# Kernel optimization log

Measured on AMD Instinct MI355X. Metric: run time of the kernel, lower is better.

## Reference

```python
import jax, jax.numpy as jnp
import numpy as np

EPS = 1e-5


def setup_inputs() -> dict:
    key = jax.random.key(0)
    ks = jax.random.split(key, 12)
    B, T, F = 8192, 512, 4
    IN = F + 1          # market features + prev_delta
    H = 32              # lstm hidden
    D1 = 32             # decision mlp width
    s = 0.1
    return {
        "x": jax.random.normal(ks[0], (B, T, F), dtype=jnp.float32),
        # BatchNorm1d (inference mode: running stats)
        "bn_gamma": jnp.ones((IN,), jnp.float32),
        "bn_beta": jnp.zeros((IN,), jnp.float32),
        "bn_mean": jnp.zeros((IN,), jnp.float32),
        "bn_var": jnp.ones((IN,), jnp.float32),
        # LSTMCell params, gate order i,f,g,o (torch convention)
        "W_ih": jax.random.normal(ks[1], (4 * H, IN), jnp.float32) * s,
        "b_ih": jax.random.normal(ks[2], (4 * H,), jnp.float32) * s,
        "W_hh": jax.random.normal(ks[3], (4 * H, H), jnp.float32) * s,
        "b_hh": jax.random.normal(ks[4], (4 * H,), jnp.float32) * s,
        # decision MLP: Linear(H,32) -> ReLU -> Linear(32,1) -> Sigmoid
        "W1": jax.random.normal(ks[5], (D1, H), jnp.float32) * s,
        "b1": jax.random.normal(ks[6], (D1,), jnp.float32) * s,
        "W2": jax.random.normal(ks[7], (1, D1), jnp.float32) * s,
        "b2": jax.random.normal(ks[8], (1,), jnp.float32) * s,
    }


def reference(x, bn_gamma, bn_beta, bn_mean, bn_var,
              W_ih, b_ih, W_hh, b_hh, W1, b1, W2, b2):
    B, T, F = x.shape
    H = W_hh.shape[1]
    inv_std = jax.lax.rsqrt(bn_var + EPS)

    def step(carry, x_t):
        h, c, d = carry                                  # [B,H],[B,H],[B,1]
        z = jnp.concatenate([x_t, d], axis=1)            # [B, F+1]
        z = (z - bn_mean) * inv_std * bn_gamma + bn_beta
        gates = z @ W_ih.T + b_ih + h @ W_hh.T + b_hh    # [B, 4H]
        i, f, g, o = jnp.split(gates, 4, axis=1)
        c = jax.nn.sigmoid(f) * c + jax.nn.sigmoid(i) * jnp.tanh(g)
        h = jax.nn.sigmoid(o) * jnp.tanh(c)
        d = jax.nn.sigmoid(jax.nn.relu(h @ W1.T + b1) @ W2.T + b2)  # [B,1]
        return (h, c, d), d

    init = (jnp.zeros((B, H), x.dtype),
            jnp.zeros((B, H), x.dtype),
            jnp.zeros((B, 1), x.dtype))
    _, deltas = jax.lax.scan(step, init, jnp.swapaxes(x, 0, 1))  # [T,B,1]
    return jnp.swapaxes(deltas, 0, 1)                             # [B,T,1]
```

## Files before the change

kernel.cpp:

```cpp
#include <hip/hip_runtime.h>
#include <math.h>

#define T_STEPS 512
#define NF 4
#define HID 32
#define BN_EPS 1e-5f
#define LOG2E 1.44269504088896340736f

typedef float    f32x2 __attribute__((ext_vector_type(2)));
typedef float    f32x4 __attribute__((ext_vector_type(4)));
typedef _Float16 f16x2 __attribute__((ext_vector_type(2)));
typedef _Float16 f16x8 __attribute__((ext_vector_type(8)));

struct F8 { f16x2 p[4]; };

__device__ __forceinline__ f16x2 pk16(float x, float y) {
  return __builtin_bit_cast(f16x2, __builtin_amdgcn_cvt_pkrtz(x, y));
}
__device__ __forceinline__ f16x8 mk8(f16x2 a, f16x2 b, f16x2 c, f16x2 d) {
  F8 f; f.p[0] = a; f.p[1] = b; f.p[2] = c; f.p[3] = d;
  return __builtin_bit_cast(f16x8, f);
}
#if __has_builtin(__builtin_amdgcn_exp2f)
__device__ __forceinline__ float ex2(float x) { return __builtin_amdgcn_exp2f(x); }
#else
__device__ __forceinline__ float ex2(float x) { return exp2f(x); }
#endif
__device__ __forceinline__ float fsigmoid(float x) {
  return __builtin_amdgcn_rcpf(1.0f + __expf(-x));
}
__device__ __forceinline__ f32x4 mfma16(f16x8 a, f16x8 b, f32x4 c) {
  return __builtin_amdgcn_mfma_f32_16x16x32_f16(a, b, c, 0, 0, 0);
}

__global__ __launch_bounds__(256, 2) void hedge_kernel(
    const float* __restrict__ x,
    const float* __restrict__ bn_g, const float* __restrict__ bn_b,
    const float* __restrict__ bn_m, const float* __restrict__ bn_v,
    const float* __restrict__ W_ih, const float* __restrict__ b_ih,
    const float* __restrict__ W_hh, const float* __restrict__ b_hh,
    const float* __restrict__ W1,   const float* __restrict__ b1,
    const float* __restrict__ W2,   const float* __restrict__ b2,
    float* __restrict__ out)
{
  __shared__ f32x4 sact[2][4][2][4][16];

  const int tid  = threadIdx.x;
  const int lane = tid & 63;
  const int w    = tid >> 6;
  const int n    = lane & 15;
  const int q    = lane >> 4;
  const int row  = blockIdx.x * 16 + n;

  float scale[5], shift[5];
  #pragma unroll
  for (int f = 0; f < 5; ++f) {
    float s = bn_g[f] * rsqrtf(bn_v[f] + BN_EPS);
    scale[f] = s;
    shift[f] = fmaf(-bn_m[f], s, bn_b[f]);
  }

  const float ke = (w == 2) ? -2.0f * LOG2E : -LOG2E;
  const float aA = (w == 2) ?  2.0f : 1.0f;
  const float bA = (w == 2) ? -1.0f : 0.0f;

  const f16x2 zz = {(_Float16)0, (_Float16)0};

  f16x8 Ahh[2], Aih[2];
  f32x4 Cb[2], Wd[2];
  #pragma unroll
  for (int pp = 0; pp < 2; ++pp) {
    const int g = 2 * w + pp;
    const float* Wr = &W_hh[(16 * g + n) * HID];
    const f32x4 lo = *(const f32x4*)&Wr[4 * q];
    const f32x4 hi = *(const f32x4*)&Wr[16 + 4 * q];
    Ahh[pp] = mk8(pk16(ke * lo.x, ke * lo.y), pk16(ke * lo.z, ke * lo.w),
                  pk16(ke * hi.x, ke * hi.y), pk16(ke * hi.z, ke * hi.w));
    const float* Wi = &W_ih[(16 * g + n) * 5];
    Aih[pp] = mk8(q == 0 ? pk16(ke * Wi[0] * scale[0], ke * Wi[1] * scale[1]) : zz,
                  q == 0 ? pk16(ke * Wi[2] * scale[2], ke * Wi[3] * scale[3]) : zz,
                  zz, zz);
    #pragma unroll
    for (int r2 = 0; r2 < 4; ++r2) {
      const int rr = 16 * g + 4 * q + r2;
      float a = b_ih[rr] + b_hh[rr];
      #pragma unroll
      for (int f = 0; f < 5; ++f) a = fmaf(W_ih[rr * 5 + f], shift[f], a);
      Cb[pp][r2] = ke * a;
      Wd[pp][r2] = ke * W_ih[rr * 5 + 4] * scale[4];
    }
  }
  f16x8 Aw1[2];
  f32x4 Cb1[2], W2v[2];
  #pragma unroll
  for (int p = 0; p < 2; ++p) {
    const float* Wr = &W1[(16 * p + n) * HID];
    const f32x4 lo = *(const f32x4*)&Wr[4 * q];
    const f32x4 hi = *(const f32x4*)&Wr[16 + 4 * q];
    Aw1[p] = mk8(pk16(lo.x, lo.y), pk16(lo.z, lo.w),
                 pk16(hi.x, hi.y), pk16(hi.z, hi.w));
    #pragma unroll
    for (int r2 = 0; r2 < 4; ++r2) {
      Cb1[p][r2] = b1[16 * p + 4 * q + r2];
      W2v[p][r2] = W2[16 * p + 4 * q + r2];
    }
  }
  const float b2s = b2[0];

  const float* xrow = x + (size_t)row * (T_STEPS * NF);
  float*       orow = out + (size_t)row * T_STEPS;

  float cst0[4] = {0, 0, 0, 0}, cst1[4] = {0, 0, 0, 0};
  f16x8 Bh = mk8(zz, zz, zz, zz);
  f32x4 xv = *(const f32x4*)xrow;

  #pragma unroll 1
  for (int t = 0; t < T_STEPS; ++t) {
    const int tn = (t + 1 < T_STEPS) ? t + 1 : t;
    const f32x4 xn = *(const f32x4*)(xrow + tn * NF);
    const int bsel = t & 1;

    const f16x8 Bz = mk8(q == 0 ? pk16(xv.x, xv.y) : zz,
                         q == 0 ? pk16(xv.z, xv.w) : zz, zz, zz);
    f32x4 D0 = mfma16(Aih[0], Bz, mfma16(Ahh[0], Bh, Cb[0]));
    f32x4 D1 = mfma16(Aih[1], Bz, mfma16(Ahh[1], Bh, Cb[1]));
    const f32x4 M0 = mfma16(Aw1[0], Bh, Cb1[0]);
    const f32x4 M1 = mfma16(Aw1[1], Bh, Cb1[1]);

    float y = 0.0f;
    #pragma unroll
    for (int r2 = 0; r2 < 4; ++r2) {
      y = fmaf(W2v[0][r2], fmaxf(M0[r2], 0.0f), y);
      y = fmaf(W2v[1][r2], fmaxf(M1[r2], 0.0f), y);
    }
    y += __builtin_bit_cast(float, __builtin_amdgcn_ds_swizzle(
             __builtin_bit_cast(int, y), 0x401F));
    y += __shfl_xor(y, 32);
    float dl = fsigmoid(y + b2s);
    dl = t ? dl : 0.0f;
    if (w == 0 && q == 0 && t) orow[t - 1] = dl;

    f32x4 A0, A1;
    #pragma unroll
    for (int r2 = 0; r2 < 4; ++r2) {
      const float d0 = fmaf(Wd[0][r2], dl, D0[r2]);
      const float d1 = fmaf(Wd[1][r2], dl, D1[r2]);
      A0[r2] = fmaf(aA, __builtin_amdgcn_rcpf(1.0f + ex2(d0)), bA);
      A1[r2] = fmaf(aA, __builtin_amdgcn_rcpf(1.0f + ex2(d1)), bA);
    }

    sact[bsel][w][0][q][n] = A0;
    sact[bsel][w][1][q][n] = A1;
    __syncthreads();
    const f32x4 Iv0 = sact[bsel][0][0][q][n], Iv1 = sact[bsel][0][1][q][n];
    const f32x4 Fv0 = sact[bsel][1][0][q][n], Fv1 = sact[bsel][1][1][q][n];
    const f32x4 Gv0 = sact[bsel][2][0][q][n], Gv1 = sact[bsel][2][1][q][n];
    const f32x4 Ov0 = sact[bsel][3][0][q][n], Ov1 = sact[bsel][3][1][q][n];

    float hN[8];
    #pragma unroll
    for (int r2 = 0; r2 < 4; ++r2) {
      float cc0 = fmaf(Fv0[r2], cst0[r2], Iv0[r2] * Gv0[r2]);
      float cc1 = fmaf(Fv1[r2], cst1[r2], Iv1[r2] * Gv1[r2]);
      cst0[r2] = cc0; cst1[r2] = cc1;
      const float tc0 = fmaf(2.0f, __builtin_amdgcn_rcpf(1.0f + ex2(-2.0f * LOG2E * cc0)), -1.0f);
      const float tc1 = fmaf(2.0f, __builtin_amdgcn_rcpf(1.0f + ex2(-2.0f * LOG2E * cc1)), -1.0f);
      hN[r2]     = Ov0[r2] * tc0;
      hN[4 + r2] = Ov1[r2] * tc1;
    }
    Bh = mk8(pk16(hN[0], hN[1]), pk16(hN[2], hN[3]),
             pk16(hN[4], hN[5]), pk16(hN[6], hN[7]));
    xv = xn;
  }

  const f32x4 M0 = mfma16(Aw1[0], Bh, Cb1[0]);
  const f32x4 M1 = mfma16(Aw1[1], Bh, Cb1[1]);
  float y = 0.0f;
  #pragma unroll
  for (int r2 = 0; r2 < 4; ++r2) {
    y = fmaf(W2v[0][r2], fmaxf(M0[r2], 0.0f), y);
    y = fmaf(W2v[1][r2], fmaxf(M1[r2], 0.0f), y);
  }
  y += __builtin_bit_cast(float, __builtin_amdgcn_ds_swizzle(
           __builtin_bit_cast(int, y), 0x401F));
  y += __shfl_xor(y, 32);
  const float dl = fsigmoid(y + b2s);
  if (w == 0 && q == 0) orow[T_STEPS - 1] = dl;
}

extern "C" void kernel_launch(void* const* d_in, const int* in_sizes, int n_in,
                              void* d_out, int out_size, void* d_ws, size_t ws_size,
                              hipStream_t stream) {
  const float* x    = (const float*)d_in[0];
  const float* bn_g = (const float*)d_in[1];
  const float* bn_b = (const float*)d_in[2];
  const float* bn_m = (const float*)d_in[3];
  const float* bn_v = (const float*)d_in[4];
  const float* W_ih = (const float*)d_in[5];
  const float* b_ih = (const float*)d_in[6];
  const float* W_hh = (const float*)d_in[7];
  const float* b_hh = (const float*)d_in[8];
  const float* W1   = (const float*)d_in[9];
  const float* b1   = (const float*)d_in[10];
  const float* W2   = (const float*)d_in[11];
  const float* b2   = (const float*)d_in[12];
  float* out = (float*)d_out;

  const int B = in_sizes[0] / (T_STEPS * NF);
  const int grid = B / 16;

  hipLaunchKernelGGL(hedge_kernel, dim3(grid), dim3(256), 0, stream,
                     x, bn_g, bn_b, bn_m, bn_v, W_ih, b_ih, W_hh, b_hh,
                     W1, b1, W2, b2, out);
}
```

Baseline: 558.7 us.

## Split LSTM gate work across eight waves and distribute the cell update per element

Doubles the block to 512 threads so each wave computes one 16-row gate slice with a single MFMA chain, where before each wave computed two. The cell and hidden update now assigns one hidden element per thread instead of eight replicated per lane. The new hidden state is exchanged through a shared buffer and re-packed into the MFMA B operand. The aim is to shorten the serial per-step critical path and raise waves per CU. The cost is a second block-wide barrier per timestep and the loss of the double-buffered activation array.

Measured after the change: 525.6 us. -5.9%, faster.

```diff
diff --git a/kernel.cpp b/kernel.cpp
--- a/kernel.cpp
+++ b/kernel.cpp
@@ -7,7 +7,6 @@
 #define BN_EPS 1e-5f
 #define LOG2E 1.44269504088896340736f
 
-typedef float    f32x2 __attribute__((ext_vector_type(2)));
 typedef float    f32x4 __attribute__((ext_vector_type(4)));
 typedef _Float16 f16x2 __attribute__((ext_vector_type(2)));
 typedef _Float16 f16x8 __attribute__((ext_vector_type(8)));
@@ -33,7 +32,7 @@
   return __builtin_amdgcn_mfma_f32_16x16x32_f16(a, b, c, 0, 0, 0);
 }
 
-__global__ __launch_bounds__(256, 2) void hedge_kernel(
+__global__ __launch_bounds__(512, 4) void hedge_kernel(
     const float* __restrict__ x,
     const float* __restrict__ bn_g, const float* __restrict__ bn_b,
     const float* __restrict__ bn_m, const float* __restrict__ bn_v,
@@ -43,7 +42,8 @@
     const float* __restrict__ W2,   const float* __restrict__ b2,
     float* __restrict__ out)
 {
-  __shared__ f32x4 sact[2][4][2][4][16];
+  __shared__ f32x4 sact[8][4][16];
+  __shared__ __align__(16) float sh[16][36];
 
   const int tid  = threadIdx.x;
   const int lane = tid & 63;
@@ -51,6 +51,7 @@
   const int n    = lane & 15;
   const int q    = lane >> 4;
   const int row  = blockIdx.x * 16 + n;
+  const int gate = w >> 1;
 
   float scale[5], shift[5];
   #pragma unroll
@@ -60,34 +61,32 @@
     shift[f] = fmaf(-bn_m[f], s, bn_b[f]);
   }
 
-  const float ke = (w == 2) ? -2.0f * LOG2E : -LOG2E;
-  const float aA = (w == 2) ?  2.0f : 1.0f;
-  const float bA = (w == 2) ? -1.0f : 0.0f;
+  const float ke = (gate == 2) ? -2.0f * LOG2E : -LOG2E;
+  const float aA = (gate == 2) ?  2.0f : 1.0f;
+  const float bA = (gate == 2) ? -1.0f : 0.0f;
 
   const f16x2 zz = {(_Float16)0, (_Float16)0};
 
-  f16x8 Ahh[2], Aih[2];
-  f32x4 Cb[2], Wd[2];
-  #pragma unroll
-  for (int pp = 0; pp < 2; ++pp) {
-    const int g = 2 * w + pp;
-    const float* Wr = &W_hh[(16 * g + n) * HID];
+  f16x8 Ahh, Aih;
+  f32x4 Cb, Wd;
+  {
+    const float* Wr = &W_hh[(16 * w + n) * HID];
     const f32x4 lo = *(const f32x4*)&Wr[4 * q];
     const f32x4 hi = *(const f32x4*)&Wr[16 + 4 * q];
-    Ahh[pp] = mk8(pk16(ke * lo.x, ke * lo.y), pk16(ke * lo.z, ke * lo.w),
-                  pk16(ke * hi.x, ke * hi.y), pk16(ke * hi.z, ke * hi.w));
-    const float* Wi = &W_ih[(16 * g + n) * 5];
-    Aih[pp] = mk8(q == 0 ? pk16(ke * Wi[0] * scale[0], ke * Wi[1] * scale[1]) : zz,
-                  q == 0 ? pk16(ke * Wi[2] * scale[2], ke * Wi[3] * scale[3]) : zz,
-                  zz, zz);
-    #pragma unroll
-    for (int r2 = 0; r2 < 4; ++r2) {
-      const int rr = 16 * g + 4 * q + r2;
+    Ahh = mk8(pk16(ke * lo.x, ke * lo.y), pk16(ke * lo.z, ke * lo.w),
+              pk16(ke * hi.x, ke * hi.y), pk16(ke * hi.z, ke * hi.w));
+    const float* Wi = &W_ih[(16 * w + n) * 5];
+    Aih = mk8(q == 0 ? pk16(ke * Wi[0] * scale[0], ke * Wi[1] * scale[1]) : zz,
+              q == 0 ? pk16(ke * Wi[2] * scale[2], ke * Wi[3] * scale[3]) : zz,
+              zz, zz);
+    #pragma unroll
+    for (int r2 = 0; r2 < 4; ++r2) {
+      const int rr = 16 * w + 4 * q + r2;
       float a = b_ih[rr] + b_hh[rr];
       #pragma unroll
       for (int f = 0; f < 5; ++f) a = fmaf(W_ih[rr * 5 + f], shift[f], a);
-      Cb[pp][r2] = ke * a;
-      Wd[pp][r2] = ke * W_ih[rr * 5 + 4] * scale[4];
+      Cb[r2] = ke * a;
+      Wd[r2] = ke * W_ih[rr * 5 + 4] * scale[4];
     }
   }
   f16x8 Aw1[2];
@@ -107,10 +106,14 @@
   }
   const float b2s = b2[0];
 
+  const float* sA   = (const float*)sact;
+  const int ibase   = (((w >> 2) * 4 + (w & 3)) * 16 + n) * 4 + q;
+  const int hwrite  = 4 * w + q;
+
   const float* xrow = x + (size_t)row * (T_STEPS * NF);
   float*       orow = out + (size_t)row * T_STEPS;
 
-  float cst0[4] = {0, 0, 0, 0}, cst1[4] = {0, 0, 0, 0};
+  float ccur = 0.0f;
   f16x8 Bh = mk8(zz, zz, zz, zz);
   f32x4 xv = *(const f32x4*)xrow;
 
@@ -118,12 +121,10 @@
   for (int t = 0; t < T_STEPS; ++t) {
     const int tn = (t + 1 < T_STEPS) ? t + 1 : t;
     const f32x4 xn = *(const f32x4*)(xrow + tn * NF);
-    const int bsel = t & 1;
 
     const f16x8 Bz = mk8(q == 0 ? pk16(xv.x, xv.y) : zz,
                          q == 0 ? pk16(xv.z, xv.w) : zz, zz, zz);
-    f32x4 D0 = mfma16(Aih[0], Bz, mfma16(Ahh[0], Bh, Cb[0]));
-    f32x4 D1 = mfma16(Aih[1], Bz, mfma16(Ahh[1], Bh, Cb[1]));
+    f32x4 D = mfma16(Aih, Bz, mfma16(Ahh, Bh, Cb));
     const f32x4 M0 = mfma16(Aw1[0], Bh, Cb1[0]);
     const f32x4 M1 = mfma16(Aw1[1], Bh, Cb1[1]);
 
@@ -140,36 +141,31 @@
     dl = t ? dl : 0.0f;
     if (w == 0 && q == 0 && t) orow[t - 1] = dl;
 
-    f32x4 A0, A1;
-    #pragma unroll
-    for (int r2 = 0; r2 < 4; ++r2) {
-      const float d0 = fmaf(Wd[0][r2], dl, D0[r2]);
-      const float d1 = fmaf(Wd[1][r2], dl, D1[r2]);
-      A0[r2] = fmaf(aA, __builtin_amdgcn_rcpf(1.0f + ex2(d0)), bA);
-      A1[r2] = fmaf(aA, __builtin_amdgcn_rcpf(1.0f + ex2(d1)), bA);
-    }
-
-    sact[bsel][w][0][q][n] = A0;
-    sact[bsel][w][1][q][n] = A1;
+    f32x4 A;
+    #pragma unroll
+    for (int r2 = 0; r2 < 4; ++r2) {
+      const float dd = fmaf(Wd[r2], dl, D[r2]);
+      A[r2] = fmaf(aA, __builtin_amdgcn_rcpf(1.0f + ex2(dd)), bA);
+    }
+
+    sact[w][q][n] = A;
     __syncthreads();
-    const f32x4 Iv0 = sact[bsel][0][0][q][n], Iv1 = sact[bsel][0][1][q][n];
-    const f32x4 Fv0 = sact[bsel][1][0][q][n], Fv1 = sact[bsel][1][1][q][n];
-    const f32x4 Gv0 = sact[bsel][2][0][q][n], Gv1 = sact[bsel][2][1][q][n];
-    const f32x4 Ov0 = sact[bsel][3][0][q][n], Ov1 = sact[bsel][3][1][q][n];
-
-    float hN[8];
-    #pragma unroll
-    for (int r2 = 0; r2 < 4; ++r2) {
-      float cc0 = fmaf(Fv0[r2], cst0[r2], Iv0[r2] * Gv0[r2]);
-      float cc1 = fmaf(Fv1[r2], cst1[r2], Iv1[r2] * Gv1[r2]);
-      cst0[r2] = cc0; cst1[r2] = cc1;
-      const float tc0 = fmaf(2.0f, __builtin_amdgcn_rcpf(1.0f + ex2(-2.0f * LOG2E * cc0)), -1.0f);
-      const float tc1 = fmaf(2.0f, __builtin_amdgcn_rcpf(1.0f + ex2(-2.0f * LOG2E * cc1)), -1.0f);
-      hN[r2]     = Ov0[r2] * tc0;
-      hN[4 + r2] = Ov1[r2] * tc1;
-    }
-    Bh = mk8(pk16(hN[0], hN[1]), pk16(hN[2], hN[3]),
-             pk16(hN[4], hN[5]), pk16(hN[6], hN[7]));
+
+    const float iv = sA[ibase];
+    const float fv = sA[ibase + 512];
+    const float gv = sA[ibase + 1024];
+    const float ov = sA[ibase + 1536];
+    const float cc = fmaf(fv, ccur, iv * gv);
+    ccur = cc;
+    const float tc = fmaf(2.0f,
+        __builtin_amdgcn_rcpf(1.0f + ex2(-2.0f * LOG2E * cc)), -1.0f);
+    sh[n][hwrite] = ov * tc;
+
+    __syncthreads();
+    const f32x4 hlo = *(const f32x4*)&sh[n][4 * q];
+    const f32x4 hhi = *(const f32x4*)&sh[n][16 + 4 * q];
+    Bh = mk8(pk16(hlo.x, hlo.y), pk16(hlo.z, hlo.w),
+             pk16(hhi.x, hhi.y), pk16(hhi.z, hhi.w));
     xv = xn;
   }
 
@@ -209,7 +205,7 @@
   const int B = in_sizes[0] / (T_STEPS * NF);
   const int grid = B / 16;
 
-  hipLaunchKernelGGL(hedge_kernel, dim3(grid), dim3(256), 0, stream,
+  hipLaunchKernelGGL(hedge_kernel, dim3(grid), dim3(512), 0, stream,
                      x, bn_g, bn_b, bn_m, bn_v, W_ih, b_ih, W_hh, b_hh,
                      W1, b1, W2, b2, out);
 }
```

## Compute all LSTM gate tiles in one wave, removing LDS exchange and barrier

Applied to the files above, without the earlier changes.

Each block is reduced from four waves to one wave, which now computes all eight gate MFMA tiles and their activations itself. This removes the per-step shared-memory exchange of gate activations and the __syncthreads barrier. In exchange, each wave does four times the MFMA and transcendental work per step, and total resident waves drop fourfold, reducing parallelism across SIMDs.

New measurement: 519.3 us. -7.1%, faster.

```diff
diff --git a/kernel.cpp b/kernel.cpp
--- a/kernel.cpp
+++ b/kernel.cpp
@@ -7,7 +7,6 @@
 #define BN_EPS 1e-5f
 #define LOG2E 1.44269504088896340736f
 
-typedef float    f32x2 __attribute__((ext_vector_type(2)));
 typedef float    f32x4 __attribute__((ext_vector_type(4)));
 typedef _Float16 f16x2 __attribute__((ext_vector_type(2)));
 typedef _Float16 f16x8 __attribute__((ext_vector_type(8)));
@@ -33,7 +32,7 @@
   return __builtin_amdgcn_mfma_f32_16x16x32_f16(a, b, c, 0, 0, 0);
 }
 
-__global__ __launch_bounds__(256, 2) void hedge_kernel(
+__global__ __launch_bounds__(64, 1) void hedge_kernel(
     const float* __restrict__ x,
     const float* __restrict__ bn_g, const float* __restrict__ bn_b,
     const float* __restrict__ bn_m, const float* __restrict__ bn_v,
@@ -43,11 +42,7 @@
     const float* __restrict__ W2,   const float* __restrict__ b2,
     float* __restrict__ out)
 {
-  __shared__ f32x4 sact[2][4][2][4][16];
-
-  const int tid  = threadIdx.x;
-  const int lane = tid & 63;
-  const int w    = tid >> 6;
+  const int lane = threadIdx.x & 63;
   const int n    = lane & 15;
   const int q    = lane >> 4;
   const int row  = blockIdx.x * 16 + n;
@@ -60,34 +55,30 @@
     shift[f] = fmaf(-bn_m[f], s, bn_b[f]);
   }
 
-  const float ke = (w == 2) ? -2.0f * LOG2E : -LOG2E;
-  const float aA = (w == 2) ?  2.0f : 1.0f;
-  const float bA = (w == 2) ? -1.0f : 0.0f;
-
   const f16x2 zz = {(_Float16)0, (_Float16)0};
 
-  f16x8 Ahh[2], Aih[2];
-  f32x4 Cb[2], Wd[2];
-  #pragma unroll
-  for (int pp = 0; pp < 2; ++pp) {
-    const int g = 2 * w + pp;
-    const float* Wr = &W_hh[(16 * g + n) * HID];
+  f16x8 Ahh[8], Aih[8];
+  f32x4 Cb[8], Wd[8];
+  #pragma unroll
+  for (int tl = 0; tl < 8; ++tl) {
+    const float ke = (tl == 4 || tl == 5) ? -2.0f * LOG2E : -LOG2E;
+    const float* Wr = &W_hh[(16 * tl + n) * HID];
     const f32x4 lo = *(const f32x4*)&Wr[4 * q];
     const f32x4 hi = *(const f32x4*)&Wr[16 + 4 * q];
-    Ahh[pp] = mk8(pk16(ke * lo.x, ke * lo.y), pk16(ke * lo.z, ke * lo.w),
+    Ahh[tl] = mk8(pk16(ke * lo.x, ke * lo.y), pk16(ke * lo.z, ke * lo.w),
                   pk16(ke * hi.x, ke * hi.y), pk16(ke * hi.z, ke * hi.w));
-    const float* Wi = &W_ih[(16 * g + n) * 5];
-    Aih[pp] = mk8(q == 0 ? pk16(ke * Wi[0] * scale[0], ke * Wi[1] * scale[1]) : zz,
+    const float* Wi = &W_ih[(16 * tl + n) * 5];
+    Aih[tl] = mk8(q == 0 ? pk16(ke * Wi[0] * scale[0], ke * Wi[1] * scale[1]) : zz,
                   q == 0 ? pk16(ke * Wi[2] * scale[2], ke * Wi[3] * scale[3]) : zz,
                   zz, zz);
     #pragma unroll
     for (int r2 = 0; r2 < 4; ++r2) {
-      const int rr = 16 * g + 4 * q + r2;
+      const int rr = 16 * tl + 4 * q + r2;
       float a = b_ih[rr] + b_hh[rr];
       #pragma unroll
       for (int f = 0; f < 5; ++f) a = fmaf(W_ih[rr * 5 + f], shift[f], a);
-      Cb[pp][r2] = ke * a;
-      Wd[pp][r2] = ke * W_ih[rr * 5 + 4] * scale[4];
+      Cb[tl][r2] = ke * a;
+      Wd[tl][r2] = ke * W_ih[rr * 5 + 4] * scale[4];
     }
   }
   f16x8 Aw1[2];
@@ -110,7 +101,7 @@
   const float* xrow = x + (size_t)row * (T_STEPS * NF);
   float*       orow = out + (size_t)row * T_STEPS;
 
-  float cst0[4] = {0, 0, 0, 0}, cst1[4] = {0, 0, 0, 0};
+  float cst[8] = {0, 0, 0, 0, 0, 0, 0, 0};
   f16x8 Bh = mk8(zz, zz, zz, zz);
   f32x4 xv = *(const f32x4*)xrow;
 
@@ -118,12 +109,13 @@
   for (int t = 0; t < T_STEPS; ++t) {
     const int tn = (t + 1 < T_STEPS) ? t + 1 : t;
     const f32x4 xn = *(const f32x4*)(xrow + tn * NF);
-    const int bsel = t & 1;
 
     const f16x8 Bz = mk8(q == 0 ? pk16(xv.x, xv.y) : zz,
                          q == 0 ? pk16(xv.z, xv.w) : zz, zz, zz);
-    f32x4 D0 = mfma16(Aih[0], Bz, mfma16(Ahh[0], Bh, Cb[0]));
-    f32x4 D1 = mfma16(Aih[1], Bz, mfma16(Ahh[1], Bh, Cb[1]));
+    f32x4 D[8];
+    #pragma unroll
+    for (int tl = 0; tl < 8; ++tl)
+      D[tl] = mfma16(Aih[tl], Bz, mfma16(Ahh[tl], Bh, Cb[tl]));
     const f32x4 M0 = mfma16(Aw1[0], Bh, Cb1[0]);
     const f32x4 M1 = mfma16(Aw1[1], Bh, Cb1[1]);
 
@@ -138,35 +130,32 @@
     y += __shfl_xor(y, 32);
     float dl = fsigmoid(y + b2s);
     dl = t ? dl : 0.0f;
-    if (w == 0 && q == 0 && t) orow[t - 1] = dl;
-
-    f32x4 A0, A1;
-    #pragma unroll
-    for (int r2 = 0; r2 < 4; ++r2) {
-      const float d0 = fmaf(Wd[0][r2], dl, D0[r2]);
-      const float d1 = fmaf(Wd[1][r2], dl, D1[r2]);
-      A0[r2] = fmaf(aA, __builtin_amdgcn_rcpf(1.0f + ex2(d0)), bA);
-      A1[r2] = fmaf(aA, __builtin_amdgcn_rcpf(1.0f + ex2(d1)), bA);
-    }
-
-    sact[bsel][w][0][q][n] = A0;
-    sact[bsel][w][1][q][n] = A1;
-    __syncthreads();
-    const f32x4 Iv0 = sact[bsel][0][0][q][n], Iv1 = sact[bsel][0][1][q][n];
-    const f32x4 Fv0 = sact[bsel][1][0][q][n], Fv1 = sact[bsel][1][1][q][n];
-    const f32x4 Gv0 = sact[bsel][2][0][q][n], Gv1 = sact[bsel][2][1][q][n];
-    const f32x4 Ov0 = sact[bsel][3][0][q][n], Ov1 = sact[bsel][3][1][q][n];
+    if (q == 0 && t) orow[t - 1] = dl;
+
+    f32x4 Ac[8];
+    #pragma unroll
+    for (int tl = 0; tl < 8; ++tl) {
+      #pragma unroll
+      for (int r2 = 0; r2 < 4; ++r2) {
+        const float dd = fmaf(Wd[tl][r2], dl, D[tl][r2]);
+        const float rc = __builtin_amdgcn_rcpf(1.0f + ex2(dd));
+        Ac[tl][r2] = (tl == 4 || tl == 5) ? fmaf(2.0f, rc, -1.0f) : rc;
+      }
+    }
 
     float hN[8];
     #pragma unroll
-    for (int r2 = 0; r2 < 4; ++r2) {
-      float cc0 = fmaf(Fv0[r2], cst0[r2], Iv0[r2] * Gv0[r2]);
-      float cc1 = fmaf(Fv1[r2], cst1[r2], Iv1[r2] * Gv1[r2]);
-      cst0[r2] = cc0; cst1[r2] = cc1;
-      const float tc0 = fmaf(2.0f, __builtin_amdgcn_rcpf(1.0f + ex2(-2.0f * LOG2E * cc0)), -1.0f);
-      const float tc1 = fmaf(2.0f, __builtin_amdgcn_rcpf(1.0f + ex2(-2.0f * LOG2E * cc1)), -1.0f);
-      hN[r2]     = Ov0[r2] * tc0;
-      hN[4 + r2] = Ov1[r2] * tc1;
+    for (int s = 0; s < 8; ++s) {
+      const int odd = s >> 2, r2 = s & 3;
+      const float iv = Ac[0 + odd][r2];
+      const float fv = Ac[2 + odd][r2];
+      const float gv = Ac[4 + odd][r2];
+      const float ov = Ac[6 + odd][r2];
+      const float cc = fmaf(fv, cst[s], iv * gv);
+      cst[s] = cc;
+      const float tc = fmaf(2.0f,
+          __builtin_amdgcn_rcpf(1.0f + ex2(-2.0f * LOG2E * cc)), -1.0f);
+      hN[s] = ov * tc;
     }
     Bh = mk8(pk16(hN[0], hN[1]), pk16(hN[2], hN[3]),
              pk16(hN[4], hN[5]), pk16(hN[6], hN[7]));
@@ -185,7 +174,7 @@
            __builtin_bit_cast(int, y), 0x401F));
   y += __shfl_xor(y, 32);
   const float dl = fsigmoid(y + b2s);
-  if (w == 0 && q == 0) orow[T_STEPS - 1] = dl;
+  if (q == 0) orow[T_STEPS - 1] = dl;
 }
 
 extern "C" void kernel_launch(void* const* d_in, const int* in_sizes, int n_in,
@@ -209,7 +198,7 @@
   const int B = in_sizes[0] / (T_STEPS * NF);
   const int grid = B / 16;
 
-  hipLaunchKernelGGL(hedge_kernel, dim3(grid), dim3(256), 0, stream,
+  hipLaunchKernelGGL(hedge_kernel, dim3(grid), dim3(64), 0, stream,
                      x, bn_g, bn_b, bn_m, bn_v, W_ih, b_ih, W_hh, b_hh,
                      W1, b1, W2, b2, out);
 }
```
